# Kernel tuning notes

Measured on AMD Instinct MI355X. Metric: run time of the kernel, lower is better.

The kernel has to match this reference:

```python
import jax, jax.numpy as jnp
import numpy as np

B, I, H = 2048, 512, 512


def _hamilton_matrix(W):
    """W: [4, O, Iin] quaternion weight components (r,i,j,k).
    Returns real block matrix M: [4*Iin, 4*O] implementing the Hamilton
    product W (*) x for component-major flattened input [r|i|j|k]."""
    Wr, Wi, Wj, Wk = W[0].T, W[1].T, W[2].T, W[3].T  # each [Iin, O]
    row_r = jnp.concatenate([Wr, Wi, Wj, Wk], axis=1)
    row_i = jnp.concatenate([-Wi, Wr, Wk, -Wj], axis=1)
    row_j = jnp.concatenate([-Wj, -Wk, Wr, Wi], axis=1)
    row_k = jnp.concatenate([-Wk, Wj, -Wi, Wr], axis=1)
    return jnp.concatenate([row_r, row_i, row_j, row_k], axis=0)


def qlinear(x, W, b=None):
    """x: [B, Iin, 4]; W: [4, O, Iin]; b: [O, 4] or None -> [B, O, 4]."""
    Bn, Iin, _ = x.shape
    O = W.shape[1]
    xf = x.transpose(0, 2, 1).reshape(Bn, 4 * Iin)  # component-major flatten
    out = xf @ _hamilton_matrix(W)                   # [B, 4*O]
    out = out.reshape(Bn, 4, O).transpose(0, 2, 1)   # [B, O, 4]
    if b is not None:
        out = out + b
    return out


def setup_inputs() -> dict:
    key = jax.random.key(0)
    ks = jax.random.split(key, 16)
    s_in = 0.02   # weight scale for numerical sanity
    d = {
        "x": jax.random.normal(ks[0], (B, I, 4), jnp.float32),
        "h": jax.random.normal(ks[1], (B, H, 4), jnp.float32),
        "c": jax.random.normal(ks[2], (B, H, 4), jnp.float32),
        "Wi_w": jax.random.normal(ks[3], (4, H, I), jnp.float32) * s_in,
        "Wf_w": jax.random.normal(ks[4], (4, H, I), jnp.float32) * s_in,
        "Wo_w": jax.random.normal(ks[5], (4, H, I), jnp.float32) * s_in,
        "Wc_w": jax.random.normal(ks[6], (4, H, I), jnp.float32) * s_in,
        "Ui_w": jax.random.normal(ks[7], (4, H, H), jnp.float32) * s_in,
        "Uf_w": jax.random.normal(ks[8], (4, H, H), jnp.float32) * s_in,
        "Uo_w": jax.random.normal(ks[9], (4, H, H), jnp.float32) * s_in,
        "Uc_w": jax.random.normal(ks[10], (4, H, H), jnp.float32) * s_in,
        "Ui_b": jax.random.normal(ks[11], (H, 4), jnp.float32) * s_in,
        "Uf_b": jax.random.normal(ks[12], (H, 4), jnp.float32) * s_in,
        "Uo_b": jax.random.normal(ks[13], (H, 4), jnp.float32) * s_in,
        "Uc_b": jax.random.normal(ks[14], (H, 4), jnp.float32) * s_in,
    }
    return d


def reference(x, h, c, Wi_w, Wf_w, Wo_w, Wc_w, Ui_w, Uf_w, Uo_w, Uc_w,
              Ui_b, Uf_b, Uo_b, Uc_b):
    # Scalar gates from real (index-0) component of quaternion gate preacts.
    i_pre = qlinear(x, Wi_w) + qlinear(h, Ui_w, Ui_b)
    f_pre = qlinear(x, Wf_w) + qlinear(h, Uf_w, Uf_b)
    o_pre = qlinear(x, Wo_w) + qlinear(h, Uo_w, Uo_b)
    c_tilde = jnp.tanh(qlinear(x, Wc_w) + qlinear(h, Uc_w, Uc_b))
    i = jax.nn.sigmoid(i_pre[..., 0])[..., None]  # [B, H, 1] broadcasts over 4 comps
    f = jax.nn.sigmoid(f_pre[..., 0])[..., None]
    o = jax.nn.sigmoid(o_pre[..., 0])[..., None]
    c_t = f * c + i * c_tilde
    h_t = o * jnp.tanh(c_t)
    return (h_t, c_t)
```

## Files before the change

kernel.cpp:

```cpp
#include <hip/hip_runtime.h>
#include <hip/hip_bf16.h>


#define BDIM 256

typedef __attribute__((ext_vector_type(8))) short short8;
typedef __attribute__((ext_vector_type(4))) float f32x4;

typedef const __attribute__((address_space(1))) void* gptr_t;
typedef __attribute__((address_space(3))) void* lptr_t;

__device__ __forceinline__ ushort f2b(float f) {
  __hip_bfloat16 h = __float2bfloat16(f);
  union { __hip_bfloat16 b; ushort u; } cv;
  cv.b = h;
  return cv.u;
}

__global__ __launch_bounds__(BDIM) void pack_kernel(
    const float* __restrict__ x, const float* __restrict__ h,
    const float* __restrict__ w0, const float* __restrict__ w1,
    const float* __restrict__ w2, const float* __restrict__ w3,
    const float* __restrict__ u0, const float* __restrict__ u1,
    const float* __restrict__ u2, const float* __restrict__ u3,
    ushort* __restrict__ A, ushort* __restrict__ Wp) {
  if (blockIdx.x < 2048) {
    int tid = blockIdx.x * BDIM + threadIdx.x;
    int b = tid >> 8;
    int pos0 = (tid & 255) << 2;
    const float* src = (pos0 < 512)
        ? (x + ((size_t)b * 512 + pos0) * 4)
        : (h + ((size_t)b * 512 + (pos0 - 512)) * 4);
    float4 q0 = reinterpret_cast<const float4*>(src)[0];
    float4 q1 = reinterpret_cast<const float4*>(src)[1];
    float4 q2 = reinterpret_cast<const float4*>(src)[2];
    float4 q3 = reinterpret_cast<const float4*>(src)[3];
    ushort* Ab = A + (size_t)b * 4096 + pos0;
    union { ushort u[4]; uint2 v; } r0, r1, r2, r3;
    r0.u[0] = f2b(q0.x); r0.u[1] = f2b(q1.x); r0.u[2] = f2b(q2.x); r0.u[3] = f2b(q3.x);
    r1.u[0] = f2b(q0.y); r1.u[1] = f2b(q1.y); r1.u[2] = f2b(q2.y); r1.u[3] = f2b(q3.y);
    r2.u[0] = f2b(q0.z); r2.u[1] = f2b(q1.z); r2.u[2] = f2b(q2.z); r2.u[3] = f2b(q3.z);
    r3.u[0] = f2b(q0.w); r3.u[1] = f2b(q1.w); r3.u[2] = f2b(q2.w); r3.u[3] = f2b(q3.w);
    *reinterpret_cast<uint2*>(Ab)        = r0.v;
    *reinterpret_cast<uint2*>(Ab + 1024) = r1.v;
    *reinterpret_cast<uint2*>(Ab + 2048) = r2.v;
    *reinterpret_cast<uint2*>(Ab + 3072) = r3.v;
  } else {
    int tid = (blockIdx.x - 2048) * BDIM + threadIdx.x;
    int n = tid >> 9;
    int k = (tid & 511) << 3;
    ushort* dst = Wp + (size_t)n * 4096 + k;
    int o = n >> 3, g = n & 7;
    if (g == 7) {
      uint4 z = {0u, 0u, 0u, 0u};
      *reinterpret_cast<uint4*>(dst) = z;
      return;
    }
    int cin = k >> 10, pos = k & 1023;
    int part = pos >> 9, ii = pos & 511;
    int gi = (g < 3) ? g : 3;
    int co = (g < 3) ? 0 : g - 3;
    int comp = cin ^ co;
    float sg = ((0x5390u >> ((cin << 2) | co)) & 1u) ? -1.0f : 1.0f;
    const float* base;
    if (part == 0) base = (gi == 0) ? w0 : (gi == 1) ? w1 : (gi == 2) ? w2 : w3;
    else           base = (gi == 0) ? u0 : (gi == 1) ? u1 : (gi == 2) ? u2 : u3;
    const float* p = base + (size_t)comp * 262144 + (size_t)o * 512 + ii;
    float4 v0 = *reinterpret_cast<const float4*>(p);
    float4 v1 = *reinterpret_cast<const float4*>(p + 4);
    union { ushort u[8]; uint4 v; } r;
    r.u[0] = f2b(sg * v0.x); r.u[1] = f2b(sg * v0.y);
    r.u[2] = f2b(sg * v0.z); r.u[3] = f2b(sg * v0.w);
    r.u[4] = f2b(sg * v1.x); r.u[5] = f2b(sg * v1.y);
    r.u[6] = f2b(sg * v1.z); r.u[7] = f2b(sg * v1.w);
    *reinterpret_cast<uint4*>(dst) = r.v;
  }
}

__global__ __launch_bounds__(BDIM, 2) void gemm_cell_kernel(
    const ushort* __restrict__ A, const ushort* __restrict__ Wp,
    const float* __restrict__ cin_, const float* __restrict__ bi,
    const float* __restrict__ bfg, const float* __restrict__ bo,
    const float* __restrict__ bc, float* __restrict__ out) {
  __shared__ ushort As[128 * 32];
  __shared__ ushort Bs[128 * 32];
  __shared__ float  Es[64 * 132];

  const int t = threadIdx.x;
  const int lane = t & 63;
  const int wid = t >> 6;
  const int wm = wid >> 1, wn = wid & 1;
  const int lrow = lane & 15;
  const int lk = (lane >> 4) << 3;
  const int m0 = blockIdx.y * 128;
  const int n0 = blockIdx.x * 128;

  f32x4 acc[4][4];
#pragma unroll
  for (int mi = 0; mi < 4; ++mi)
#pragma unroll
    for (int ni = 0; ni < 4; ++ni)
      acc[mi][ni] = (f32x4){0.f, 0.f, 0.f, 0.f};

  const int rA = t >> 2;
  const int cA = (t & 3) << 3;
  const ushort* Abase = A + (size_t)m0 * 4096;
  const ushort* Bbase = Wp + (size_t)n0 * 4096;

  for (int kt = 0; kt < 4096; kt += 32) {
#pragma unroll
    for (int ch = 0; ch < 2; ++ch) {
      const ushort* ga = Abase + (size_t)(ch * 64 + rA) * 4096 + kt + cA;
      const ushort* gb = Bbase + (size_t)(ch * 64 + rA) * 4096 + kt + cA;
      __builtin_amdgcn_global_load_lds((gptr_t)ga, (lptr_t)(As + ch * 2048 + t * 8),
                                       16, 0, 0);
      __builtin_amdgcn_global_load_lds((gptr_t)gb, (lptr_t)(Bs + ch * 2048 + t * 8),
                                       16, 0, 0);
    }
    __syncthreads();
    short8 a[4], b[4];
#pragma unroll
    for (int f = 0; f < 4; ++f) {
      a[f] = *reinterpret_cast<const short8*>(As + (wm * 64 + f * 16 + lrow) * 32 + lk);
      b[f] = *reinterpret_cast<const short8*>(Bs + (wn * 64 + f * 16 + lrow) * 32 + lk);
    }
#pragma unroll
    for (int mi = 0; mi < 4; ++mi)
#pragma unroll
      for (int ni = 0; ni < 4; ++ni)
        acc[mi][ni] = __builtin_amdgcn_mfma_f32_16x16x32_bf16(
            a[mi], b[ni], acc[mi][ni], 0, 0, 0);
    __syncthreads();
  }

  const int o0 = blockIdx.x * 16;
  const int lr4 = (lane >> 4) << 2;

#pragma unroll
  for (int ch = 0; ch < 2; ++ch) {
    if (wm == ch) {
#pragma unroll
      for (int mi = 0; mi < 4; ++mi)
#pragma unroll
        for (int ni = 0; ni < 4; ++ni) {
          float* dst = Es + (mi * 16 + lr4) * 132 + wn * 64 + ni * 16 + lrow;
#pragma unroll
          for (int r = 0; r < 4; ++r) dst[r * 132] = acc[mi][ni][r];
        }
    }
    __syncthreads();
#pragma unroll
    for (int i = 0; i < 4; ++i) {
      int p = t + i * 256;
      int bl = p >> 4;
      int ol = p & 15;
      const float* e = Es + bl * 132 + ol * 8;
      int b = m0 + ch * 64 + bl;
      int o = o0 + ol;
      float4 bcv = *reinterpret_cast<const float4*>(bc + (size_t)o * 4);
      float ip = e[0] + bi[o << 2];
      float fp = e[1] + bfg[o << 2];
      float op = e[2] + bo[o << 2];
      float g0 = tanhf(e[3] + bcv.x);
      float g1 = tanhf(e[4] + bcv.y);
      float g2 = tanhf(e[5] + bcv.z);
      float g3 = tanhf(e[6] + bcv.w);
      float ig = 1.f / (1.f + expf(-ip));
      float fg = 1.f / (1.f + expf(-fp));
      float og = 1.f / (1.f + expf(-op));
      float4 cv = *reinterpret_cast<const float4*>(cin_ + ((size_t)b * 512 + o) * 4);
      float4 ct, ht;
      ct.x = fg * cv.x + ig * g0;  ht.x = og * tanhf(ct.x);
      ct.y = fg * cv.y + ig * g1;  ht.y = og * tanhf(ct.y);
      ct.z = fg * cv.z + ig * g2;  ht.z = og * tanhf(ct.z);
      ct.w = fg * cv.w + ig * g3;  ht.w = og * tanhf(ct.w);
      *reinterpret_cast<float4*>(out + ((size_t)b * 512 + o) * 4) = ht;
      *reinterpret_cast<float4*>(out + 4194304 + ((size_t)b * 512 + o) * 4) = ct;
    }
    __syncthreads();
  }
}

extern "C" void kernel_launch(void* const* d_in, const int* in_sizes, int n_in,
                              void* d_out, int out_size, void* d_ws, size_t ws_size,
                              hipStream_t stream) {
  const float* x   = (const float*)d_in[0];
  const float* h   = (const float*)d_in[1];
  const float* c   = (const float*)d_in[2];
  const float* wi  = (const float*)d_in[3];
  const float* wf  = (const float*)d_in[4];
  const float* wo  = (const float*)d_in[5];
  const float* wc  = (const float*)d_in[6];
  const float* ui  = (const float*)d_in[7];
  const float* uf  = (const float*)d_in[8];
  const float* uo  = (const float*)d_in[9];
  const float* uc  = (const float*)d_in[10];
  const float* bi  = (const float*)d_in[11];
  const float* bf_ = (const float*)d_in[12];
  const float* bo  = (const float*)d_in[13];
  const float* bc  = (const float*)d_in[14];
  float* out = (float*)d_out;

  ushort* A  = (ushort*)d_ws;
  ushort* Wp = (ushort*)((char*)d_ws + (size_t)16777216);

  hipLaunchKernelGGL(pack_kernel, dim3(10240), dim3(BDIM), 0, stream,
                     x, h, wi, wf, wo, wc, ui, uf, uo, uc, A, Wp);
  hipLaunchKernelGGL(gemm_cell_kernel, dim3(32, 16), dim3(BDIM), 0, stream,
                     A, Wp, c, bi, bf_, bo, bc, out);
}
```

Baseline: 240.5 us.

## Triple-buffer GEMM with swizzled LDS, larger 128x256 tiles, and XCD-aware block mapping

The GEMM kernel grows to 512 threads with a 128x256 tile and a BK of 64. It uses a three-stage global_load_lds pipeline with prefetch two steps ahead and a single barrier per iteration, plus s_setprio around the MFMA bursts. The pack kernel XOR-swizzles the A and W layouts so the LDS fragment reads avoid bank conflicts. A 1D grid is remapped so each XCD gets a contiguous sub-block for L2 reuse. This adds more LDS per block (144KB), which risks lower occupancy, and it depends on the pack and GEMM swizzles staying consistent.

New measurement: 214.3 us. 10.9% less time.

```diff
diff --git a/kernel.cpp b/kernel.cpp
--- a/kernel.cpp
+++ b/kernel.cpp
@@ -3,6 +3,7 @@
 
 
 #define BDIM 256
+#define GDIM 512
 
 typedef __attribute__((ext_vector_type(8))) short short8;
 typedef __attribute__((ext_vector_type(4))) float f32x4;
@@ -35,7 +36,8 @@
     float4 q1 = reinterpret_cast<const float4*>(src)[1];
     float4 q2 = reinterpret_cast<const float4*>(src)[2];
     float4 q3 = reinterpret_cast<const float4*>(src)[3];
-    ushort* Ab = A + (size_t)b * 4096 + pos0;
+    int swz = (b & 7) << 3;
+    ushort* Ab = A + (size_t)b * 4096 + (pos0 ^ swz);
     union { ushort u[4]; uint2 v; } r0, r1, r2, r3;
     r0.u[0] = f2b(q0.x); r0.u[1] = f2b(q1.x); r0.u[2] = f2b(q2.x); r0.u[3] = f2b(q3.x);
     r1.u[0] = f2b(q0.y); r1.u[1] = f2b(q1.y); r1.u[2] = f2b(q2.y); r1.u[3] = f2b(q3.y);
@@ -49,7 +51,8 @@
     int tid = (blockIdx.x - 2048) * BDIM + threadIdx.x;
     int n = tid >> 9;
     int k = (tid & 511) << 3;
-    ushort* dst = Wp + (size_t)n * 4096 + k;
+    int swz = (n & 7) << 3;
+    ushort* dst = Wp + (size_t)n * 4096 + (k ^ swz);
     int o = n >> 3, g = n & 7;
     if (g == 7) {
       uint4 z = {0u, 0u, 0u, 0u};
@@ -77,23 +80,31 @@
   }
 }
 
-__global__ __launch_bounds__(BDIM, 2) void gemm_cell_kernel(
+__global__ __launch_bounds__(GDIM, 2) void gemm_cell_kernel(
     const ushort* __restrict__ A, const ushort* __restrict__ Wp,
     const float* __restrict__ cin_, const float* __restrict__ bi,
     const float* __restrict__ bfg, const float* __restrict__ bo,
     const float* __restrict__ bc, float* __restrict__ out) {
-  __shared__ ushort As[128 * 32];
-  __shared__ ushort Bs[128 * 32];
-  __shared__ float  Es[64 * 132];
+  __shared__ ushort SMEM[73728];
+  ushort* As = SMEM;
+  ushort* Bs = SMEM + 24576;
 
   const int t = threadIdx.x;
   const int lane = t & 63;
   const int wid = t >> 6;
-  const int wm = wid >> 1, wn = wid & 1;
+  const int wm = wid >> 2;
+  const int wn = wid & 3;
   const int lrow = lane & 15;
-  const int lk = (lane >> 4) << 3;
-  const int m0 = blockIdx.y * 128;
-  const int n0 = blockIdx.x * 128;
+  const int lk8 = (lane >> 4) << 3;
+  const int swzE = (lrow & 7) << 3;
+
+  const int bid = blockIdx.x;
+  const int xcd = bid & 7;
+  const int loc = bid >> 3;
+  const int bx = (xcd & 1) * 8 + (loc & 7);
+  const int by = (xcd >> 1) * 4 + (loc >> 3);
+  const int m0 = by * 128;
+  const int n0 = bx * 256;
 
   f32x4 acc[4][4];
 #pragma unroll
@@ -102,83 +113,135 @@
     for (int ni = 0; ni < 4; ++ni)
       acc[mi][ni] = (f32x4){0.f, 0.f, 0.f, 0.f};
 
-  const int rA = t >> 2;
-  const int cA = (t & 3) << 3;
-  const ushort* Abase = A + (size_t)m0 * 4096;
-  const ushort* Bbase = Wp + (size_t)n0 * 4096;
-
-  for (int kt = 0; kt < 4096; kt += 32) {
-#pragma unroll
-    for (int ch = 0; ch < 2; ++ch) {
-      const ushort* ga = Abase + (size_t)(ch * 64 + rA) * 4096 + kt + cA;
-      const ushort* gb = Bbase + (size_t)(ch * 64 + rA) * 4096 + kt + cA;
-      __builtin_amdgcn_global_load_lds((gptr_t)ga, (lptr_t)(As + ch * 2048 + t * 8),
-                                       16, 0, 0);
-      __builtin_amdgcn_global_load_lds((gptr_t)gb, (lptr_t)(Bs + ch * 2048 + t * 8),
-                                       16, 0, 0);
-    }
-    __syncthreads();
-    short8 a[4], b[4];
-#pragma unroll
-    for (int f = 0; f < 4; ++f) {
-      a[f] = *reinterpret_cast<const short8*>(As + (wm * 64 + f * 16 + lrow) * 32 + lk);
-      b[f] = *reinterpret_cast<const short8*>(Bs + (wn * 64 + f * 16 + lrow) * 32 + lk);
-    }
-#pragma unroll
-    for (int mi = 0; mi < 4; ++mi)
+  const ushort* Ag = A + (size_t)m0 * 4096;
+  const ushort* Bg = Wp + (size_t)n0 * 4096;
+  const int c8 = (t & 7) << 3;
+
+#define STAGE_A(KT, S, I)                                                     \
+  {                                                                           \
+    int j = t + (I) * 512;                                                    \
+    __builtin_amdgcn_global_load_lds(                                         \
+        (gptr_t)(Ag + (size_t)(j >> 3) * 4096 + (KT) * 64 + c8),              \
+        (lptr_t)(As + (S) * 8192 + j * 8), 16, 0, 0);                         \
+  }
+#define STAGE_B(KT, S, I)                                                     \
+  {                                                                           \
+    int j = t + (I) * 512;                                                    \
+    __builtin_amdgcn_global_load_lds(                                         \
+        (gptr_t)(Bg + (size_t)(j >> 3) * 4096 + (KT) * 64 + c8),              \
+        (lptr_t)(Bs + (S) * 16384 + j * 8), 16, 0, 0);                        \
+  }
+
+  STAGE_A(0, 0, 0) STAGE_A(0, 0, 1)
+  STAGE_B(0, 0, 0) STAGE_B(0, 0, 1) STAGE_B(0, 0, 2) STAGE_B(0, 0, 3)
+  STAGE_A(1, 1, 0) STAGE_A(1, 1, 1)
+  STAGE_B(1, 1, 0) STAGE_B(1, 1, 1) STAGE_B(1, 1, 2) STAGE_B(1, 1, 3)
+  asm volatile("s_waitcnt vmcnt(6)" ::: "memory");
+  __builtin_amdgcn_s_barrier();
+  __builtin_amdgcn_sched_barrier(0);
+
+  int cur = 0;
+  for (int kt = 0; kt < 64; ++kt) {
+    const int pf = (kt < 62);
+    const int ps = (cur >= 1) ? cur - 1 : 2;
+    const ushort* Ac = As + cur * 8192;
+    const ushort* Bc = Bs + cur * 16384;
+
+    {
+      const int c0 = lk8 ^ swzE;
+      short8 af[4], bf[4];
+#pragma unroll
+      for (int mi = 0; mi < 4; ++mi)
+        af[mi] = *reinterpret_cast<const short8*>(Ac + (wm * 64 + mi * 16 + lrow) * 64 + c0);
 #pragma unroll
       for (int ni = 0; ni < 4; ++ni)
-        acc[mi][ni] = __builtin_amdgcn_mfma_f32_16x16x32_bf16(
-            a[mi], b[ni], acc[mi][ni], 0, 0, 0);
-    __syncthreads();
-  }
-
-  const int o0 = blockIdx.x * 16;
+        bf[ni] = *reinterpret_cast<const short8*>(Bc + (wn * 64 + ni * 16 + lrow) * 64 + c0);
+      if (pf) { STAGE_A(kt + 2, ps, 0) STAGE_A(kt + 2, ps, 1) STAGE_B(kt + 2, ps, 0) }
+      __builtin_amdgcn_s_setprio(1);
+#pragma unroll
+      for (int mi = 0; mi < 4; ++mi)
+#pragma unroll
+        for (int ni = 0; ni < 4; ++ni)
+          acc[mi][ni] = __builtin_amdgcn_mfma_f32_16x16x32_bf16(
+              af[mi], bf[ni], acc[mi][ni], 0, 0, 0);
+      __builtin_amdgcn_s_setprio(0);
+    }
+    {
+      const int c1 = (32 + lk8) ^ swzE;
+      short8 af[4], bf[4];
+#pragma unroll
+      for (int mi = 0; mi < 4; ++mi)
+        af[mi] = *reinterpret_cast<const short8*>(Ac + (wm * 64 + mi * 16 + lrow) * 64 + c1);
+#pragma unroll
+      for (int ni = 0; ni < 4; ++ni)
+        bf[ni] = *reinterpret_cast<const short8*>(Bc + (wn * 64 + ni * 16 + lrow) * 64 + c1);
+      if (pf) { STAGE_B(kt + 2, ps, 1) STAGE_B(kt + 2, ps, 2) STAGE_B(kt + 2, ps, 3) }
+      __builtin_amdgcn_s_setprio(1);
+#pragma unroll
+      for (int mi = 0; mi < 4; ++mi)
+#pragma unroll
+        for (int ni = 0; ni < 4; ++ni)
+          acc[mi][ni] = __builtin_amdgcn_mfma_f32_16x16x32_bf16(
+              af[mi], bf[ni], acc[mi][ni], 0, 0, 0);
+      __builtin_amdgcn_s_setprio(0);
+    }
+
+    if (kt < 62)       { asm volatile("s_waitcnt vmcnt(6)" ::: "memory"); }
+    else if (kt == 62) { asm volatile("s_waitcnt vmcnt(0)" ::: "memory"); }
+    __builtin_amdgcn_s_barrier();
+    __builtin_amdgcn_sched_barrier(0);
+    cur = (cur == 2) ? 0 : cur + 1;
+  }
+  __syncthreads();
+
+  float* Es = (float*)SMEM;
+  const int o0 = bx * 32;
   const int lr4 = (lane >> 4) << 2;
 
 #pragma unroll
-  for (int ch = 0; ch < 2; ++ch) {
-    if (wm == ch) {
-#pragma unroll
-      for (int mi = 0; mi < 4; ++mi)
+  for (int wmc = 0; wmc < 2; ++wmc) {
+#pragma unroll
+    for (int mi = 0; mi < 4; ++mi) {
+      if (wm == wmc) {
 #pragma unroll
         for (int ni = 0; ni < 4; ++ni) {
-          float* dst = Es + (mi * 16 + lr4) * 132 + wn * 64 + ni * 16 + lrow;
-#pragma unroll
-          for (int r = 0; r < 4; ++r) dst[r * 132] = acc[mi][ni][r];
+          float* dst = Es + lr4 * 260 + wn * 64 + ni * 16 + lrow;
+#pragma unroll
+          for (int r = 0; r < 4; ++r) dst[r * 260] = acc[mi][ni][r];
         }
-    }
-    __syncthreads();
-#pragma unroll
-    for (int i = 0; i < 4; ++i) {
-      int p = t + i * 256;
-      int bl = p >> 4;
-      int ol = p & 15;
-      const float* e = Es + bl * 132 + ol * 8;
-      int b = m0 + ch * 64 + bl;
-      int o = o0 + ol;
-      float4 bcv = *reinterpret_cast<const float4*>(bc + (size_t)o * 4);
-      float ip = e[0] + bi[o << 2];
-      float fp = e[1] + bfg[o << 2];
-      float op = e[2] + bo[o << 2];
-      float g0 = tanhf(e[3] + bcv.x);
-      float g1 = tanhf(e[4] + bcv.y);
-      float g2 = tanhf(e[5] + bcv.z);
-      float g3 = tanhf(e[6] + bcv.w);
-      float ig = 1.f / (1.f + expf(-ip));
-      float fg = 1.f / (1.f + expf(-fp));
-      float og = 1.f / (1.f + expf(-op));
-      float4 cv = *reinterpret_cast<const float4*>(cin_ + ((size_t)b * 512 + o) * 4);
-      float4 ct, ht;
-      ct.x = fg * cv.x + ig * g0;  ht.x = og * tanhf(ct.x);
-      ct.y = fg * cv.y + ig * g1;  ht.y = og * tanhf(ct.y);
-      ct.z = fg * cv.z + ig * g2;  ht.z = og * tanhf(ct.z);
-      ct.w = fg * cv.w + ig * g3;  ht.w = og * tanhf(ct.w);
-      *reinterpret_cast<float4*>(out + ((size_t)b * 512 + o) * 4) = ht;
-      *reinterpret_cast<float4*>(out + 4194304 + ((size_t)b * 512 + o) * 4) = ct;
-    }
-    __syncthreads();
-  }
+      }
+      __syncthreads();
+      {
+        int bl = t >> 5;
+        int ol = t & 31;
+        const float* e = Es + bl * 260 + ol * 8;
+        int b = m0 + wmc * 64 + mi * 16 + bl;
+        int o = o0 + ol;
+        float4 bcv = *reinterpret_cast<const float4*>(bc + (size_t)o * 4);
+        float ip = e[0] + bi[o << 2];
+        float fp = e[1] + bfg[o << 2];
+        float op = e[2] + bo[o << 2];
+        float g0 = tanhf(e[3] + bcv.x);
+        float g1 = tanhf(e[4] + bcv.y);
+        float g2 = tanhf(e[5] + bcv.z);
+        float g3 = tanhf(e[6] + bcv.w);
+        float ig = 1.f / (1.f + expf(-ip));
+        float fg = 1.f / (1.f + expf(-fp));
+        float og = 1.f / (1.f + expf(-op));
+        float4 cv = *reinterpret_cast<const float4*>(cin_ + ((size_t)b * 512 + o) * 4);
+        float4 ct, ht;
+        ct.x = fg * cv.x + ig * g0;  ht.x = og * tanhf(ct.x);
+        ct.y = fg * cv.y + ig * g1;  ht.y = og * tanhf(ct.y);
+        ct.z = fg * cv.z + ig * g2;  ht.z = og * tanhf(ct.z);
+        ct.w = fg * cv.w + ig * g3;  ht.w = og * tanhf(ct.w);
+        *reinterpret_cast<float4*>(out + ((size_t)b * 512 + o) * 4) = ht;
+        *reinterpret_cast<float4*>(out + 4194304 + ((size_t)b * 512 + o) * 4) = ct;
+      }
+      __syncthreads();
+    }
+  }
+#undef STAGE_A
+#undef STAGE_B
 }
 
 extern "C" void kernel_launch(void* const* d_in, const int* in_sizes, int n_in,
@@ -206,6 +269,6 @@
 
   hipLaunchKernelGGL(pack_kernel, dim3(10240), dim3(BDIM), 0, stream,
                      x, h, wi, wf, wo, wc, ui, uf, uo, uc, A, Wp);
-  hipLaunchKernelGGL(gemm_cell_kernel, dim3(32, 16), dim3(BDIM), 0, stream,
+  hipLaunchKernelGGL(gemm_cell_kernel, dim3(256), dim3(GDIM), 0, stream,
                      A, Wp, c, bi, bf_, bo, bc, out);
 }
```
